# Optimization experiments

Hardware: AMD Instinct MI355X
Metric: run time of the kernel (lower is better)

The kernel has to match this reference:

```python
import jax, jax.numpy as jnp
import numpy as np

# Hyperparameters matching the torch module instantiation
STRIDE = (2, 2, 2)
PADDING = (1, 1, 1)
OUTPUT_PADDING = (1, 1, 1)
DILATION = (2, 2, 2)
KERNEL = (3, 3, 3)


def setup_inputs() -> dict:
    key = jax.random.key(0)
    k1, k2, k3 = jax.random.split(key, 3)
    x = jax.random.normal(k1, (2, 64, 32, 32, 32), dtype=jnp.float32)
    # torch ConvTranspose3d weight layout: (C_in, C_out//groups, kD, kH, kW)
    weight = jax.random.normal(k2, (64, 32, 3, 3, 3), dtype=jnp.float32) * 0.05
    bias = jax.random.normal(k3, (32,), dtype=jnp.float32) * 0.05
    return {"x": x, "weight": weight, "bias": bias}


def reference(x, weight, bias):
    # Same math as the naive torch module: zero-insertion upsample by stride,
    # symmetric pad by dilation*(k-1)-padding, dense conv3d with the spatially
    # flipped weight at rhs dilation, trailing output_padding, then bias add.
    # lhs_dilation performs the zero-insertion implicitly (identical result).
    pad = tuple(max(0, d * (k - 1) - p)
                for d, k, p in zip(DILATION, KERNEL, PADDING))
    # (C_in, C_out, k,k,k) -> (C_out, C_in, k,k,k), flipped spatially
    w = jnp.flip(jnp.transpose(weight, (1, 0, 2, 3, 4)), axis=(2, 3, 4))
    out = jax.lax.conv_general_dilated(
        x, w,
        window_strides=(1, 1, 1),
        padding=[(p, p) for p in pad],
        lhs_dilation=STRIDE,
        rhs_dilation=DILATION,
        dimension_numbers=("NCDHW", "OIDHW", "NCDHW"),
    )
    opd, oph, opw = OUTPUT_PADDING
    out = jnp.pad(out, ((0, 0), (0, 0), (0, opd), (0, oph), (0, opw)))
    return out + bias[None, :, None, None, None]
```

## Files before the change

### kernel.cpp

```cpp
#include <hip/hip_runtime.h>


#define DOUT 66
#define PL (DOUT*DOUT)

typedef _Float16 half8 __attribute__((ext_vector_type(8)));
typedef float    floatx16 __attribute__((ext_vector_type(16)));

#define X16_N_F16  2228224
#define ROW_B      4352
#define ZSLAB_OFF  112640
#define X16_OFF    131072

__global__ void w_prep(const float* __restrict__ w, _Float16* __restrict__ wA) {
    int o = blockIdx.x * 256 + threadIdx.x;
    if (o >= 55296) return;
    int j = o & 7;
    int tmp = o >> 3;
    int lane = tmp & 63;
    int g = tmp >> 6;
    int cc = g / 27, tap = g - cc * 27;
    int co = lane & 31, khalf = lane >> 5;
    int ci = cc * 16 + khalf * 8 + j;
    wA[o] = (_Float16)w[ci * 864 + co * 27 + tap];
}

__global__ void x_to_f16t(const float* __restrict__ x, _Float16* __restrict__ x16,
                          uint4* __restrict__ zslab) {
    const int tid = threadIdx.x;
    const unsigned b = blockIdx.x;
    const int id  = b & 31;
    const int ihg = (b >> 5) & 3;
    const int n   = b >> 7;
    const int iw  = tid & 31;
    const int ih  = ihg * 8 + (tid >> 5);

    if (b == 0) {
        zslab[2 * tid]     = make_uint4(0, 0, 0, 0);
        zslab[2 * tid + 1] = make_uint4(0, 0, 0, 0);
    }

    const float* xr = x + (size_t)n * 2097152 + (id * 32 + ih) * 32 + iw;
    _Float16* drow = x16 + (size_t)n * X16_N_F16 + (id * 32 + ih) * 2176;

    #pragma unroll
    for (int c0 = 0; c0 < 64; c0 += 16) {
        float f[16];
        #pragma unroll
        for (int j = 0; j < 16; ++j) f[j] = xr[(size_t)(c0 + j) * 32768];
        unsigned pk[8];
        #pragma unroll
        for (int j = 0; j < 8; ++j)
            pk[j] = __builtin_bit_cast(unsigned,
                        __builtin_amdgcn_cvt_pkrtz(f[2 * j], f[2 * j + 1]));
        const int ccg0 = c0 >> 3;
        *(uint4*)(drow + ccg0 * 272 + (iw + 1) * 8) =
            make_uint4(pk[0], pk[1], pk[2], pk[3]);
        *(uint4*)(drow + (ccg0 + 1) * 272 + (iw + 1) * 8) =
            make_uint4(pk[4], pk[5], pk[6], pk[7]);
    }
    if (tid < 128) {
        const int ihq = tid >> 4;
        const int rem = tid & 15;
        const int ccg = rem >> 1, side = rem & 1;
        _Float16* hz = x16 + (size_t)n * X16_N_F16 +
                       (id * 32 + ihg * 8 + ihq) * 2176 + ccg * 272 + (side ? 264 : 0);
        *(uint4*)hz = make_uint4(0, 0, 0, 0);
    }
}

#define BIAS_TOT4 (2*32*34*(PL/4))
__global__ void bias_planes(const float* __restrict__ bias, float* __restrict__ out) {
    const int tid = threadIdx.x;
    const unsigned base = blockIdx.x * 4096u;
    #pragma unroll
    for (int j = 0; j < 16; ++j) {
        unsigned idx = base + j * 256u + tid;
        if (idx >= BIAS_TOT4) continue;
        unsigned pl = idx / 1089u;
        unsigned slot = idx - pl * 1089u;
        unsigned e  = pl % 34u;
        unsigned nc = pl / 34u;
        unsigned od = (e < 33u) ? 2u * e : 65u;
        float v = bias[nc & 31u];
        float4* p = (float4*)(out + ((size_t)nc * DOUT + od) * PL);
        p[slot] = make_float4(v, v, v, v);
    }
}

__global__ void __launch_bounds__(256, 2) convt_mfma(
    const _Float16* __restrict__ x16, const _Float16* __restrict__ wA,
    const _Float16* __restrict__ zslab, const float* __restrict__ bias,
    float* __restrict__ out)
{
    __shared__ __align__(16) unsigned char xlds[78848];

    const int tid  = threadIdx.x;
    const int lane = tid & 63;
    const int wv   = tid >> 6;

    unsigned b = blockIdx.x;
    const unsigned xcd = b & 7u;
    const int n   = xcd & 1;
    const int dp  = (b >> 3) & 31;
    const int hq  = b >> 8;
    const int hpg = (int)(((xcd >> 1) << 1) | hq);
    const int hpb = hpg * 4;

    uint4 A[27];
    const _Float16* wl = wA + ((size_t)wv * 27 * 64 + lane) * 8;
    #pragma unroll
    for (int t = 0; t < 27; ++t) A[t] = *(const uint4*)(wl + t * 512);

    const char* xby = (const char*)(x16 + (size_t)n * X16_N_F16);
    const char* zby = (const char*)zslab;
    for (int m = wv; m < 77; m += 4) {
        int c = m * 64 + lane;
        int r = c / 272;
        int q = c - r * 272;
        const char* g;
        if (r < 18) {
            int idl = r / 6, ihl = r - idl * 6;
            int id = dp - 1 + idl, ih = hpb - 1 + ihl;
            bool v = ((unsigned)id < 32u) & ((unsigned)ih < 32u);
            g = v ? (xby + (id * 32 + ih) * ROW_B + q * 16) : (zby + q * 16);
        } else {
            g = zby;
        }
        __builtin_amdgcn_global_load_lds(
            (const __attribute__((address_space(1))) void*)g,
            (__attribute__((address_space(3))) void*)(xlds + m * 1024),
            16, 0, 0);
    }
    __syncthreads();

    const int wp    = lane & 31;
    const int khalf = lane >> 5;
    const int cbase = (2 * wv + khalf) * 544 + wp * 16;

    floatx16 acc[4] = {{}, {}, {}, {}};
    #pragma unroll
    for (int kd = 0; kd < 3; ++kd)
    #pragma unroll
    for (int kh = 0; kh < 3; ++kh)
    #pragma unroll
    for (int kw = 0; kw < 3; ++kw) {
        const int tap = (kd * 3 + kh) * 3 + kw;
        #pragma unroll
        for (int t = 0; t < 4; ++t) {
            const int row = (2 - kd) * 6 + (t + 2 - kh);
            const uint4* bp = (const uint4*)(xlds + row * ROW_B + cbase + (2 - kw) * 16);
            acc[t] = __builtin_amdgcn_mfma_f32_32x32x16_f16(
                __builtin_bit_cast(half8, A[tap]),
                __builtin_bit_cast(half8, *bp), acc[t], 0, 0, 0);
        }
    }

    __syncthreads();
    float* part = (float*)xlds;
    if (wv > 0) {
        #pragma unroll
        for (int t = 0; t < 4; ++t)
            #pragma unroll
            for (int r = 0; r < 16; ++r)
                part[((wv - 1) * 64 + t * 16 + r) * 64 + lane] = acc[t][r];
    }
    __syncthreads();

    const int od = 2 * dp + 1;
    if (wv == 0) {
        #pragma unroll
        for (int t = 0; t < 4; ++t) {
            const int oh = 2 * (hpb + t) + 1;
            #pragma unroll
            for (int r = 0; r < 16; ++r) {
                float s = acc[t][r]
                    + part[(t * 16 + r) * 64 + lane]
                    + part[(64 + t * 16 + r) * 64 + lane]
                    + part[(128 + t * 16 + r) * 64 + lane];
                const int co = (r & 3) + 8 * (r >> 2) + 4 * khalf;
                const float bv = bias[co];
                float2* orow = (float2*)(out +
                    ((size_t)(n * 32 + co) * DOUT + od) * PL + oh * DOUT);
                orow[wp] = make_float2(bv, s + bv);
                if (wp == 31) orow[32] = make_float2(bv, bv);
            }
        }
    } else if (wv <= 2) {
        #pragma unroll
        for (int tt = 0; tt < 2; ++tt) {
            const int oh = 2 * (hpb + (wv - 1) * 2 + tt);
            #pragma unroll
            for (int r = 0; r < 16; ++r) {
                const int co = (r & 3) + 8 * (r >> 2) + 4 * khalf;
                const float bv = bias[co];
                float2* erow = (float2*)(out +
                    ((size_t)(n * 32 + co) * DOUT + od) * PL + oh * DOUT);
                erow[wp] = make_float2(bv, bv);
                if (wp == 31) erow[32] = make_float2(bv, bv);
            }
        }
    } else if (hpg == 7) {
        #pragma unroll
        for (int tt = 0; tt < 2; ++tt) {
            const int oh = 64 + tt;
            #pragma unroll
            for (int r = 0; r < 16; ++r) {
                const int co = (r & 3) + 8 * (r >> 2) + 4 * khalf;
                const float bv = bias[co];
                float2* erow = (float2*)(out +
                    ((size_t)(n * 32 + co) * DOUT + od) * PL + oh * DOUT);
                erow[wp] = make_float2(bv, bv);
                if (wp == 31) erow[32] = make_float2(bv, bv);
            }
        }
    }
}

extern "C" void kernel_launch(void* const* d_in, const int* in_sizes, int n_in,
                              void* d_out, int out_size, void* d_ws, size_t ws_size,
                              hipStream_t stream) {
    const float* x    = (const float*)d_in[0];
    const float* wgt  = (const float*)d_in[1];
    const float* bias = (const float*)d_in[2];
    float* out = (float*)d_out;
    _Float16* wA    = (_Float16*)d_ws;
    uint4*    zslab = (uint4*)((char*)d_ws + ZSLAB_OFF);
    _Float16* x16   = (_Float16*)((char*)d_ws + X16_OFF);

    w_prep<<<216, 256, 0, stream>>>(wgt, wA);
    x_to_f16t<<<256, 256, 0, stream>>>(x, x16, zslab);
    bias_planes<<<(BIAS_TOT4 + 4095) / 4096, 256, 0, stream>>>(bias, out);
    convt_mfma<<<512, 256, 0, stream>>>(x16, wA, (const _Float16*)zslab, bias, out);
}
```

Measured before the change: 110.8 us.

## Fuse prep kernels into one launch and balance conv epilogue reduction across waves

Merges the weight conversion, input fp16 transpose and bias-fill kernels into a single block-partitioned prep kernel, which cuts two launches. The bias-only even-row writes in odd depth planes move from the conv kernel into the prep kernel. The conv epilogue now has every wave reduce and store one output row, where wave 0 used to do all the reduction while the others wrote bias rows. Weight register loads are issued after the async LDS loads so the two overlap. In exchange the prep kernel does more scattered small stores, and the larger x-transpose grid adds register pressure from 32 floats per thread.

```diff
diff --git a/kernel.cpp b/kernel.cpp
--- a/kernel.cpp
+++ b/kernel.cpp
@@ -12,79 +12,111 @@
 #define ZSLAB_OFF  112640
 #define X16_OFF    131072
 
-__global__ void w_prep(const float* __restrict__ w, _Float16* __restrict__ wA) {
-    int o = blockIdx.x * 256 + threadIdx.x;
-    if (o >= 55296) return;
-    int j = o & 7;
-    int tmp = o >> 3;
-    int lane = tmp & 63;
-    int g = tmp >> 6;
-    int cc = g / 27, tap = g - cc * 27;
-    int co = lane & 31, khalf = lane >> 5;
-    int ci = cc * 16 + khalf * 8 + j;
-    wA[o] = (_Float16)w[ci * 864 + co * 27 + tap];
-}
-
-__global__ void x_to_f16t(const float* __restrict__ x, _Float16* __restrict__ x16,
-                          uint4* __restrict__ zslab) {
+#define PB_W    216
+#define PB_X    512
+#define PB_BA   579
+#define PB_BB   561
+#define PREP_GRID (PB_W + PB_X + PB_BA + PB_BB)
+
+__global__ void __launch_bounds__(256) prep(
+    const float* __restrict__ x, const float* __restrict__ w,
+    const float* __restrict__ bias, _Float16* __restrict__ wA,
+    _Float16* __restrict__ x16, uint4* __restrict__ zslab,
+    float* __restrict__ out)
+{
     const int tid = threadIdx.x;
-    const unsigned b = blockIdx.x;
-    const int id  = b & 31;
-    const int ihg = (b >> 5) & 3;
-    const int n   = b >> 7;
-    const int iw  = tid & 31;
-    const int ih  = ihg * 8 + (tid >> 5);
-
-    if (b == 0) {
-        zslab[2 * tid]     = make_uint4(0, 0, 0, 0);
-        zslab[2 * tid + 1] = make_uint4(0, 0, 0, 0);
-    }
-
-    const float* xr = x + (size_t)n * 2097152 + (id * 32 + ih) * 32 + iw;
-    _Float16* drow = x16 + (size_t)n * X16_N_F16 + (id * 32 + ih) * 2176;
-
-    #pragma unroll
-    for (int c0 = 0; c0 < 64; c0 += 16) {
-        float f[16];
-        #pragma unroll
-        for (int j = 0; j < 16; ++j) f[j] = xr[(size_t)(c0 + j) * 32768];
-        unsigned pk[8];
-        #pragma unroll
-        for (int j = 0; j < 8; ++j)
-            pk[j] = __builtin_bit_cast(unsigned,
-                        __builtin_amdgcn_cvt_pkrtz(f[2 * j], f[2 * j + 1]));
-        const int ccg0 = c0 >> 3;
-        *(uint4*)(drow + ccg0 * 272 + (iw + 1) * 8) =
-            make_uint4(pk[0], pk[1], pk[2], pk[3]);
-        *(uint4*)(drow + (ccg0 + 1) * 272 + (iw + 1) * 8) =
-            make_uint4(pk[4], pk[5], pk[6], pk[7]);
-    }
-    if (tid < 128) {
-        const int ihq = tid >> 4;
-        const int rem = tid & 15;
-        const int ccg = rem >> 1, side = rem & 1;
-        _Float16* hz = x16 + (size_t)n * X16_N_F16 +
-                       (id * 32 + ihg * 8 + ihq) * 2176 + ccg * 272 + (side ? 264 : 0);
-        *(uint4*)hz = make_uint4(0, 0, 0, 0);
-    }
-}
-
-#define BIAS_TOT4 (2*32*34*(PL/4))
-__global__ void bias_planes(const float* __restrict__ bias, float* __restrict__ out) {
-    const int tid = threadIdx.x;
-    const unsigned base = blockIdx.x * 4096u;
-    #pragma unroll
-    for (int j = 0; j < 16; ++j) {
-        unsigned idx = base + j * 256u + tid;
-        if (idx >= BIAS_TOT4) continue;
-        unsigned pl = idx / 1089u;
-        unsigned slot = idx - pl * 1089u;
-        unsigned e  = pl % 34u;
-        unsigned nc = pl / 34u;
-        unsigned od = (e < 33u) ? 2u * e : 65u;
-        float v = bias[nc & 31u];
-        float4* p = (float4*)(out + ((size_t)nc * DOUT + od) * PL);
-        p[slot] = make_float4(v, v, v, v);
+    unsigned b = blockIdx.x;
+
+    if (b < PB_W) {
+        int o = b * 256 + tid;
+        int j = o & 7;
+        int tmp = o >> 3;
+        int lane = tmp & 63;
+        int g = tmp >> 6;
+        int cc = g / 27, tap = g - cc * 27;
+        int co = lane & 31, khalf = lane >> 5;
+        int ci = cc * 16 + khalf * 8 + j;
+        wA[o] = (_Float16)w[ci * 864 + co * 27 + tap];
+        return;
+    }
+    b -= PB_W;
+    if (b < PB_X) {
+        const int id = b & 31;
+        const int q2 = (b >> 5) & 7;
+        const int n  = b >> 8;
+        const int iw = tid & 31;
+        const int cihalf = (tid >> 5) & 1;
+        const int ihq = tid >> 6;
+        const int ih = q2 * 4 + ihq;
+
+        if (b == 0 && tid < 256) {
+            zslab[2 * tid]     = make_uint4(0, 0, 0, 0);
+            zslab[2 * tid + 1] = make_uint4(0, 0, 0, 0);
+        }
+
+        const float* xr = x + (size_t)n * 2097152 + (id * 32 + ih) * 32 + iw;
+        _Float16* drow = x16 + (size_t)n * X16_N_F16 + (id * 32 + ih) * 2176;
+        const int c0 = cihalf * 32;
+
+        float f[32];
+        #pragma unroll
+        for (int j = 0; j < 32; ++j) f[j] = xr[(size_t)(c0 + j) * 32768];
+        #pragma unroll
+        for (int k = 0; k < 4; ++k) {
+            unsigned pk[4];
+            #pragma unroll
+            for (int j = 0; j < 4; ++j)
+                pk[j] = __builtin_bit_cast(unsigned,
+                    __builtin_amdgcn_cvt_pkrtz(f[8 * k + 2 * j], f[8 * k + 2 * j + 1]));
+            const int ccg = cihalf * 4 + k;
+            *(uint4*)(drow + ccg * 272 + (iw + 1) * 8) =
+                make_uint4(pk[0], pk[1], pk[2], pk[3]);
+        }
+        if (tid < 64) {
+            const int ihq2 = tid >> 4;
+            const int rem  = tid & 15;
+            const int ccg  = rem >> 1, side = rem & 1;
+            _Float16* hz = x16 + (size_t)n * X16_N_F16 +
+                (id * 32 + q2 * 4 + ihq2) * 2176 + ccg * 272 + (side ? 264 : 0);
+            *(uint4*)hz = make_uint4(0, 0, 0, 0);
+        }
+        return;
+    }
+    b -= PB_X;
+    if (b < PB_BA) {
+        const unsigned base = b * 4096u;
+        #pragma unroll
+        for (int j = 0; j < 16; ++j) {
+            unsigned idx = base + j * 256u + tid;
+            if (idx >= 2369952u) continue;
+            unsigned pl = idx / 1089u;
+            unsigned slot = idx - pl * 1089u;
+            unsigned e  = pl % 34u;
+            unsigned nc = pl / 34u;
+            unsigned od = (e < 33u) ? 2u * e : 65u;
+            float v = bias[nc & 31u];
+            float4* p = (float4*)(out + ((size_t)nc * DOUT + od) * PL);
+            p[slot] = make_float4(v, v, v, v);
+        }
+        return;
+    }
+    b -= PB_BA;
+    {
+        const unsigned base = b * 4096u;
+        #pragma unroll
+        for (int j = 0; j < 16; ++j) {
+            unsigned idx = base + j * 256u + tid;
+            unsigned slot = idx % 33u;
+            unsigned t2   = idx / 33u;
+            unsigned rr   = t2 % 34u;
+            unsigned pln  = t2 / 34u;
+            unsigned oh = (rr < 33u) ? 2u * rr : 65u;
+            unsigned od = 2u * (pln & 31u) + 1u;
+            unsigned nc = pln >> 5;
+            float v = bias[nc & 31u];
+            float2* p = (float2*)(out + ((size_t)nc * DOUT + od) * PL + oh * DOUT);
+            p[slot] = make_float2(v, v);
+        }
     }
 }
 
@@ -106,11 +138,6 @@
     const int hq  = b >> 8;
     const int hpg = (int)(((xcd >> 1) << 1) | hq);
     const int hpb = hpg * 4;
-
-    uint4 A[27];
-    const _Float16* wl = wA + ((size_t)wv * 27 * 64 + lane) * 8;
-    #pragma unroll
-    for (int t = 0; t < 27; ++t) A[t] = *(const uint4*)(wl + t * 512);
 
     const char* xby = (const char*)(x16 + (size_t)n * X16_N_F16);
     const char* zby = (const char*)zslab;
@@ -132,6 +159,12 @@
             (__attribute__((address_space(3))) void*)(xlds + m * 1024),
             16, 0, 0);
     }
+
+    uint4 A[27];
+    const _Float16* wl = wA + ((size_t)wv * 27 * 64 + lane) * 8;
+    #pragma unroll
+    for (int t = 0; t < 27; ++t) A[t] = *(const uint4*)(wl + t * 512);
+
     __syncthreads();
 
     const int wp    = lane & 31;
@@ -158,62 +191,36 @@
 
     __syncthreads();
     float* part = (float*)xlds;
-    if (wv > 0) {
-        #pragma unroll
-        for (int t = 0; t < 4; ++t)
-            #pragma unroll
-            for (int r = 0; r < 16; ++r)
-                part[((wv - 1) * 64 + t * 16 + r) * 64 + lane] = acc[t][r];
+    #pragma unroll
+    for (int t = 0; t < 4; ++t) {
+        if (t == wv) continue;
+        #pragma unroll
+        for (int r = 0; r < 16; ++r)
+            part[((t * 4 + wv) * 16 + r) * 64 + lane] = acc[t][r];
     }
     __syncthreads();
 
+    float s[16];
+    #pragma unroll
+    for (int r = 0; r < 16; ++r) s[r] = acc[wv][r];
+    #pragma unroll
+    for (int w2 = 0; w2 < 4; ++w2) {
+        if (w2 == wv) continue;
+        #pragma unroll
+        for (int r = 0; r < 16; ++r)
+            s[r] += part[((wv * 4 + w2) * 16 + r) * 64 + lane];
+    }
+
     const int od = 2 * dp + 1;
-    if (wv == 0) {
-        #pragma unroll
-        for (int t = 0; t < 4; ++t) {
-            const int oh = 2 * (hpb + t) + 1;
-            #pragma unroll
-            for (int r = 0; r < 16; ++r) {
-                float s = acc[t][r]
-                    + part[(t * 16 + r) * 64 + lane]
-                    + part[(64 + t * 16 + r) * 64 + lane]
-                    + part[(128 + t * 16 + r) * 64 + lane];
-                const int co = (r & 3) + 8 * (r >> 2) + 4 * khalf;
-                const float bv = bias[co];
-                float2* orow = (float2*)(out +
-                    ((size_t)(n * 32 + co) * DOUT + od) * PL + oh * DOUT);
-                orow[wp] = make_float2(bv, s + bv);
-                if (wp == 31) orow[32] = make_float2(bv, bv);
-            }
-        }
-    } else if (wv <= 2) {
-        #pragma unroll
-        for (int tt = 0; tt < 2; ++tt) {
-            const int oh = 2 * (hpb + (wv - 1) * 2 + tt);
-            #pragma unroll
-            for (int r = 0; r < 16; ++r) {
-                const int co = (r & 3) + 8 * (r >> 2) + 4 * khalf;
-                const float bv = bias[co];
-                float2* erow = (float2*)(out +
-                    ((size_t)(n * 32 + co) * DOUT + od) * PL + oh * DOUT);
-                erow[wp] = make_float2(bv, bv);
-                if (wp == 31) erow[32] = make_float2(bv, bv);
-            }
-        }
-    } else if (hpg == 7) {
-        #pragma unroll
-        for (int tt = 0; tt < 2; ++tt) {
-            const int oh = 64 + tt;
-            #pragma unroll
-            for (int r = 0; r < 16; ++r) {
-                const int co = (r & 3) + 8 * (r >> 2) + 4 * khalf;
-                const float bv = bias[co];
-                float2* erow = (float2*)(out +
-                    ((size_t)(n * 32 + co) * DOUT + od) * PL + oh * DOUT);
-                erow[wp] = make_float2(bv, bv);
-                if (wp == 31) erow[32] = make_float2(bv, bv);
-            }
-        }
+    const int oh = 2 * (hpb + wv) + 1;
+    #pragma unroll
+    for (int r = 0; r < 16; ++r) {
+        const int co = (r & 3) + 8 * (r >> 2) + 4 * khalf;
+        const float bv = bias[co];
+        float2* orow = (float2*)(out +
+            ((size_t)(n * 32 + co) * DOUT + od) * PL + oh * DOUT);
+        orow[wp] = make_float2(bv, s[r] + bv);
+        if (wp == 31) orow[32] = make_float2(bv, bv);
     }
 }
 
@@ -228,8 +235,6 @@
     uint4*    zslab = (uint4*)((char*)d_ws + ZSLAB_OFF);
     _Float16* x16   = (_Float16*)((char*)d_ws + X16_OFF);
 
-    w_prep<<<216, 256, 0, stream>>>(wgt, wA);
-    x_to_f16t<<<256, 256, 0, stream>>>(x, x16, zslab);
-    bias_planes<<<(BIAS_TOT4 + 4095) / 4096, 256, 0, stream>>>(bias, out);
+    prep<<<PREP_GRID, 256, 0, stream>>>(x, wgt, bias, wA, x16, zslab, out);
     convt_mfma<<<512, 256, 0, stream>>>(x16, wA, (const _Float16*)zslab, bias, out);
 }
```

Result: slower. 118.0 us (+6.5%).
